# Kernel tuning notes

Measured on AMD Instinct MI355X. Metric: run time of the kernel, lower is better.

The kernel has to match this reference:

```python
import jax, jax.numpy as jnp
import numpy as np

N_NODES = 100000
N_EDGES = 1600000
D_IN = 128
D_HID = 128
D_OUT = 128


def setup_inputs() -> dict:
    key = jax.random.key(0)
    ks = jax.random.split(key, 6)
    node_features = jax.random.normal(ks[0], (N_NODES, D_IN), dtype=jnp.float32)
    edge_index = jax.random.randint(ks[1], (2, N_EDGES), 0, N_NODES, dtype=jnp.int32)
    s1 = 1.0 / np.sqrt(D_IN)
    s2 = 1.0 / np.sqrt(D_HID)
    W1 = jax.random.normal(ks[2], (D_IN, D_HID), dtype=jnp.float32) * s1
    W2 = jax.random.normal(ks[3], (D_HID, D_HID), dtype=jnp.float32) * s2
    W3 = jax.random.normal(ks[4], (D_HID, D_OUT), dtype=jnp.float32) * s2
    b1 = jnp.zeros((D_HID,), dtype=jnp.float32)
    b2 = jnp.zeros((D_HID,), dtype=jnp.float32)
    b3 = jnp.zeros((D_OUT,), dtype=jnp.float32)
    return {"node_features": node_features, "edge_index": edge_index,
            "W1": W1, "b1": b1, "W2": W2, "b2": b2, "W3": W3, "b3": b3}


def _aggregate(x, src, dst, n_nodes):
    # mean over incoming neighbors (by dst), residual add; degree clamped to >=1
    msg = jax.ops.segment_sum(x[src], dst, num_segments=n_nodes)  # [N, D]
    deg = jax.ops.segment_sum(jnp.ones_like(dst, dtype=x.dtype), dst,
                              num_segments=n_nodes)
    deg = jnp.maximum(deg, 1.0)[:, None]
    return x + msg / deg


def reference(node_features, edge_index, W1, b1, W2, b2, W3, b3):
    n_nodes = node_features.shape[0]
    src, dst = edge_index[0], edge_index[1]
    x = _aggregate(node_features, src, dst, n_nodes)
    x = jax.nn.relu(x @ W1 + b1)
    x = _aggregate(x, src, dst, n_nodes)
    x = jax.nn.relu(x @ W2 + b2)
    x = x.mean(axis=0)  # graph readout -> [D_HID]
    return x @ W3 + b3  # [D_OUT]
```

## Files before the change

### kernel.cpp

```cpp
#include <hip/hip_runtime.h>

#define D 128
#define SLOTS 64
#define NB 391
#define NBANK 4
#define SUBCAP 1536
#define BINCAP (NBANK * SUBCAP)
#define BATCH 2048
#define EPB 8
#define CNTSTRIDE 16
#define WPITCH 136

typedef __attribute__((ext_vector_type(8))) short short8;
typedef __attribute__((ext_vector_type(4))) float float4v;

__device__ inline unsigned short f2bf(float f) {
    union { float f; unsigned u; } a; a.f = f;
    unsigned u = a.u;
    return (unsigned short)((u + 0x7fffu + ((u >> 16) & 1u)) >> 16);
}
__device__ inline unsigned packbf(float a, float b) {
    return (unsigned)f2bf(a) | ((unsigned)f2bf(b) << 16);
}
__device__ inline unsigned pack4fp8(float a, float b, float c, float d) {
    int t = __builtin_amdgcn_cvt_pk_fp8_f32(a, b, 0, false);
    t = __builtin_amdgcn_cvt_pk_fp8_f32(c, d, t, true);
    return (unsigned)t;
}
__device__ inline unsigned char pack1fp8(float a) {
    int t = __builtin_amdgcn_cvt_pk_fp8_f32(a, 0.f, 0, false);
    return (unsigned char)(t & 0xff);
}
__device__ inline void acc8fp8(float* acc, uint2 w) {
    auto f0 = __builtin_amdgcn_cvt_pk_f32_fp8(w.x, false);
    auto f1 = __builtin_amdgcn_cvt_pk_f32_fp8(w.x, true);
    auto f2 = __builtin_amdgcn_cvt_pk_f32_fp8(w.y, false);
    auto f3 = __builtin_amdgcn_cvt_pk_f32_fp8(w.y, true);
    acc[0] += f0[0]; acc[1] += f0[1]; acc[2] += f1[0]; acc[3] += f1[1];
    acc[4] += f2[0]; acc[5] += f2[1]; acc[6] += f3[0]; acc[7] += f3[1];
}


__global__ __launch_bounds__(256) void k_head(const int* __restrict__ src,
                                              const int* __restrict__ dst, int nE,
                                              int* __restrict__ gcnt, int* __restrict__ bins,
                                              const float* __restrict__ x,
                                              unsigned char* __restrict__ y8,
                                              unsigned char* __restrict__ h8dummy,
                                              float* __restrict__ colsum,
                                              int n16, int nBatches) {
    __shared__ int hist[512];
    __shared__ int excl[512];
    __shared__ int base[NB];
    __shared__ int stage[BATCH];
    __shared__ int gofs[BATCH];
    __shared__ int waveSum[4];
    int tid = threadIdx.x;

    if (blockIdx.x >= nBatches) {
        int cb = blockIdx.x - nBatches;
        if (cb == 0) {
            if (tid < 128) colsum[tid] = 0.f;
            else if (tid < 136)
                reinterpret_cast<uint4*>(y8)[(size_t)n16 + (tid - 128)] = make_uint4(0, 0, 0, 0);
            else if (tid < 144)
                reinterpret_cast<uint4*>(h8dummy)[tid - 136] = make_uint4(0, 0, 0, 0);
        }
        int i = cb * 256 + tid;
        if (i < n16) {
            const float4* xin = reinterpret_cast<const float4*>(x) + (size_t)i * 4;
            float4 v0 = xin[0], v1 = xin[1], v2 = xin[2], v3 = xin[3];
            uint4 o;
            o.x = pack4fp8(v0.x, v0.y, v0.z, v0.w);
            o.y = pack4fp8(v1.x, v1.y, v1.z, v1.w);
            o.z = pack4fp8(v2.x, v2.y, v2.z, v2.w);
            o.w = pack4fp8(v3.x, v3.y, v3.z, v3.w);
            reinterpret_cast<uint4*>(y8)[i] = o;
        }
        return;
    }

    int start = blockIdx.x * BATCH;
    int cntB = nE - start; if (cntB > BATCH) cntB = BATCH;
    if (cntB <= 0) return;
    int bank = blockIdx.x & (NBANK - 1);

    hist[tid] = 0; hist[tid + 256] = 0;
    __syncthreads();

    int b[EPB], r[EPB], v[EPB];
    #pragma unroll
    for (int i = 0; i < EPB; ++i) {
        int e = start + i * 256 + tid;
        if (e < nE) {
            int d = dst[e];
            b[i] = d >> 8;
            v[i] = (src[e] << 8) | (d & 255);
            r[i] = atomicAdd(&hist[b[i]], 1);
        } else b[i] = -1;
    }
    __syncthreads();

    int e0 = tid * 2, e1 = e0 + 1;
    int h0 = hist[e0], h1v = hist[e1];
    int s = h0 + h1v;
    int lane = tid & 63, w = tid >> 6;
    int sum = s;
    #pragma unroll
    for (int off2 = 1; off2 < 64; off2 <<= 1) {
        int tmp = __shfl_up(sum, off2, 64);
        if (lane >= off2) sum += tmp;
    }
    if (lane == 63) waveSum[w] = sum;
    __syncthreads();
    int wbase = 0;
    if (w > 0) wbase += waveSum[0];
    if (w > 1) wbase += waveSum[1];
    if (w > 2) wbase += waveSum[2];
    int exclPair = wbase + sum - s;
    excl[e0] = exclPair;
    excl[e1] = exclPair + h0;
    if (tid < NB)
        base[tid] = atomicAdd(&gcnt[(tid * NBANK + bank) * CNTSTRIDE], hist[tid]);
    if (tid + 256 < NB)
        base[tid + 256] = atomicAdd(&gcnt[((tid + 256) * NBANK + bank) * CNTSTRIDE], hist[tid + 256]);
    __syncthreads();

    #pragma unroll
    for (int i = 0; i < EPB; ++i) {
        if (b[i] >= 0) {
            int p = excl[b[i]] + r[i];
            int o = base[b[i]] + r[i];
            stage[p] = v[i];
            gofs[p] = (o < SUBCAP) ? (b[i] * BINCAP + bank * SUBCAP + o) : -1;
        }
    }
    __syncthreads();

    #pragma unroll
    for (int i = 0; i < EPB; ++i) {
        int p = i * 256 + tid;
        if (p < cntB) {
            int g = gofs[p];
            if (g >= 0) bins[g] = stage[p];
        }
    }
}


__global__ __launch_bounds__(256) void k_scatter2(const int* __restrict__ gcnt,
                                                  const int* __restrict__ bins,
                                                  int* __restrict__ slots,
                                                  int* __restrict__ deg, int n, int nAll) {
    __shared__ int slotsL[128 * SLOTS];
    __shared__ int cntL[128];
    __shared__ int cnt4s[128];
    int tid = threadIdx.x;
    int bin = blockIdx.x >> 1;
    int half = blockIdx.x & 1;
    if (tid < 128) cntL[tid] = 0;
    __syncthreads();

    #pragma unroll
    for (int k = 0; k < NBANK; ++k) {
        int c = gcnt[(bin * NBANK + k) * CNTSTRIDE]; if (c > SUBCAP) c = SUBCAP;
        const int* eb = bins + (size_t)bin * BINCAP + k * SUBCAP;
        for (int i = tid; i < c; i += 256) {
            int vv = eb[i];
            int dl = vv & 255;
            if ((dl >> 7) == half) {
                int p = atomicAdd(&cntL[dl & 127], 1);
                if (p < SLOTS) slotsL[(dl & 127) * SLOTS + p] = vv >> 8;
            }
        }
    }
    __syncthreads();

    int node0 = bin * 256 + half * 128;
    int remNodes = n - node0;
    if (remNodes > 128) remNodes = 128;
    if (remNodes < 0) remNodes = 0;

    if (tid < remNodes) {
        int dg = cntL[tid]; if (dg > SLOTS) dg = SLOTS;
        int dgr = (dg + 3) & ~3;
        for (int p = dg; p < dgr; ++p) slotsL[tid * SLOTS + p] = nAll;
        deg[node0 + tid] = dg;
        cnt4s[tid] = dgr;
    }
    __syncthreads();

    uint4* gout = reinterpret_cast<uint4*>(slots + (size_t)node0 * SLOTS);
    const uint4* lin = reinterpret_cast<const uint4*>(slotsL);
    int nv = remNodes * (SLOTS / 4);
    for (int i = tid; i < nv; i += 256) {
        int nd = i >> 4, vec = i & 15;
        if ((vec << 2) < cnt4s[nd]) gout[i] = lin[i];
    }
}


__global__ void k_agg(const unsigned char* __restrict__ Xin8,
                      unsigned short* __restrict__ Xout,
                      const int* __restrict__ deg, const int* __restrict__ slots, int n) {
    int t = blockIdx.x * 256 + threadIdx.x;
    int node = t >> 4;
    int lane = t & 15;
    if (node >= n) return;
    int dg = deg[node];
    int cnt4 = (dg + 3) & ~3;
    float acc[8] = {0.f, 0.f, 0.f, 0.f, 0.f, 0.f, 0.f, 0.f};
    const int* sl = slots + (size_t)node * SLOTS;
    for (int j = 0; j < cnt4; j += 4) {
        int4 s4 = *reinterpret_cast<const int4*>(sl + j);
        uint2 w0 = *reinterpret_cast<const uint2*>(Xin8 + (size_t)s4.x * D + lane * 8);
        uint2 w1 = *reinterpret_cast<const uint2*>(Xin8 + (size_t)s4.y * D + lane * 8);
        uint2 w2 = *reinterpret_cast<const uint2*>(Xin8 + (size_t)s4.z * D + lane * 8);
        uint2 w3 = *reinterpret_cast<const uint2*>(Xin8 + (size_t)s4.w * D + lane * 8);
        acc8fp8(acc, w0); acc8fp8(acc, w1); acc8fp8(acc, w2); acc8fp8(acc, w3);
    }
    float inv = 1.0f / (float)(dg > 0 ? dg : 1);
    uint2 s8 = *reinterpret_cast<const uint2*>(Xin8 + (size_t)node * D + lane * 8);
    float self[8] = {0.f, 0.f, 0.f, 0.f, 0.f, 0.f, 0.f, 0.f};
    acc8fp8(self, s8);
    float o[8];
    #pragma unroll
    for (int k = 0; k < 8; ++k) o[k] = self[k] + acc[k] * inv;
    uint4 ov;
    ov.x = packbf(o[0], o[1]); ov.y = packbf(o[2], o[3]);
    ov.z = packbf(o[4], o[5]); ov.w = packbf(o[6], o[7]);
    reinterpret_cast<uint4*>(Xout + (size_t)node * D)[lane] = ov;
}


__global__ __launch_bounds__(256) void k_gemm(const unsigned short* __restrict__ X,
                                              const float* __restrict__ W,
                                              const float* __restrict__ bias,
                                              unsigned char* __restrict__ Y8,
                                              float* __restrict__ colsum,
                                              int n, int mode) {
    __shared__ unsigned short Wt[128 * WPITCH];
    __shared__ float cs[128];
    int tid = threadIdx.x;
    int wave = tid >> 6, L = tid & 63;
    int m16 = L & 15, g = L >> 4;

    #pragma unroll
    for (int i = 0; i < 8; ++i) {
        int p = i * 256 + tid;
        int col = p & 127, kg = p >> 7;
        unsigned pk[4];
        #pragma unroll
        for (int h = 0; h < 4; ++h) {
            float w0 = W[(kg * 8 + 2 * h + 0) * 128 + col];
            float w1 = W[(kg * 8 + 2 * h + 1) * 128 + col];
            pk[h] = packbf(w0, w1);
        }
        *reinterpret_cast<uint4*>(&Wt[col * WPITCH + kg * 8]) =
            make_uint4(pk[0], pk[1], pk[2], pk[3]);
    }
    if (mode && tid < 128) cs[tid] = 0.f;
    __syncthreads();

    int row0 = blockIdx.x * 128 + wave * 32;
    float4v zero4 = {0.f, 0.f, 0.f, 0.f};
    float4v acc[2][8];
    #pragma unroll
    for (int rt = 0; rt < 2; ++rt)
        #pragma unroll
        for (int ct = 0; ct < 8; ++ct) acc[rt][ct] = zero4;

    #pragma unroll
    for (int q = 0; q < 4; ++q) {
        int k0 = q * 32;
        short8 a[2];
        #pragma unroll
        for (int rt = 0; rt < 2; ++rt) {
            int row = row0 + rt * 16 + m16;
            short8 af = {0, 0, 0, 0, 0, 0, 0, 0};
            if (row < n)
                af = *reinterpret_cast<const short8*>(X + (size_t)row * D + k0 + g * 8);
            a[rt] = af;
        }
        #pragma unroll
        for (int ct = 0; ct < 8; ++ct) {
            short8 b = *reinterpret_cast<const short8*>(&Wt[(ct * 16 + m16) * WPITCH + k0 + g * 8]);
            acc[0][ct] = __builtin_amdgcn_mfma_f32_16x16x32_bf16(a[0], b, acc[0][ct], 0, 0, 0);
            acc[1][ct] = __builtin_amdgcn_mfma_f32_16x16x32_bf16(a[1], b, acc[1][ct], 0, 0, 0);
        }
    }

    float bj[8];
    #pragma unroll
    for (int ct = 0; ct < 8; ++ct) bj[ct] = bias[ct * 16 + m16];

    if (mode == 0) {
        #pragma unroll
        for (int rt = 0; rt < 2; ++rt)
            #pragma unroll
            for (int i = 0; i < 4; ++i) {
                int row = row0 + rt * 16 + g * 4 + i;
                if (row < n) {
                    #pragma unroll
                    for (int ct = 0; ct < 8; ++ct) {
                        float v = fmaxf(acc[rt][ct][i] + bj[ct], 0.f);
                        Y8[(size_t)row * D + ct * 16 + m16] = pack1fp8(v);
                    }
                }
            }
    } else {
        float csv[8] = {0.f, 0.f, 0.f, 0.f, 0.f, 0.f, 0.f, 0.f};
        #pragma unroll
        for (int rt = 0; rt < 2; ++rt)
            #pragma unroll
            for (int i = 0; i < 4; ++i) {
                int row = row0 + rt * 16 + g * 4 + i;
                if (row < n) {
                    #pragma unroll
                    for (int ct = 0; ct < 8; ++ct)
                        csv[ct] += fmaxf(acc[rt][ct][i] + bj[ct], 0.f);
                }
            }
        #pragma unroll
        for (int ct = 0; ct < 8; ++ct) atomicAdd(&cs[ct * 16 + m16], csv[ct]);
        __syncthreads();
        if (tid < 128) atomicAdd(&colsum[tid], cs[tid]);
    }
}


__global__ void k_final(const float* __restrict__ colsum, const float* __restrict__ W3,
                        const float* __restrict__ b3, float* __restrict__ out, float invN) {
    int j = threadIdx.x;
    float acc = b3[j];
    #pragma unroll 8
    for (int k = 0; k < D; ++k)
        acc += colsum[k] * invN * W3[k * D + j];
    out[j] = acc;
}


extern "C" void kernel_launch(void* const* d_in, const int* in_sizes, int n_in,
                              void* d_out, int out_size, void* d_ws, size_t ws_size,
                              hipStream_t stream) {
    const float* nf = (const float*)d_in[0];
    const int*   ei = (const int*)d_in[1];
    const float* W1 = (const float*)d_in[2];
    const float* b1 = (const float*)d_in[3];
    const float* W2 = (const float*)d_in[4];
    const float* b2 = (const float*)d_in[5];
    const float* W3 = (const float*)d_in[6];
    const float* b3 = (const float*)d_in[7];
    float* out = (float*)d_out;

    int n  = in_sizes[0] / D;
    int nE = in_sizes[1] / 2;
    const int* src = ei;
    const int* dst = ei + nE;

    int nBins = (n + 255) / 256;
    int nBatches = (nE + BATCH - 1) / BATCH;
    int n16 = n * (D / 16);

    char* ws = (char*)d_ws;
    size_t off = 0;
    auto alloc = [&](size_t bytes) -> void* {
        off = (off + 255) & ~(size_t)255;
        void* p = ws + off;
        off += bytes;
        return p;
    };
    int* gcnt  = (int*)alloc((size_t)nBins * NBANK * CNTSTRIDE * 4);
    int* bins  = (int*)alloc((size_t)nBins * BINCAP * 4);
    int* slots = (int*)alloc((size_t)nBins * 256 * SLOTS * 4);
    int* deg   = (int*)alloc((size_t)n * 4);
    unsigned char*  x8  = (unsigned char*) alloc((size_t)(n + 1) * D);
    unsigned short* t16 = (unsigned short*)alloc((size_t)n * D * 2);
    unsigned char*  h8  = (unsigned char*) alloc((size_t)(n + 1) * D);
    float* colsum = (float*)alloc(128 * 4);

    hipMemsetAsync(gcnt, 0, (size_t)nBins * NBANK * CNTSTRIDE * 4, stream);

    int gC = (n16 + 255) / 256;
    int gA = (n * 16 + 255) / 256;
    int gG = (n + 127) / 128;

    k_head<<<nBatches + gC, 256, 0, stream>>>(src, dst, nE, gcnt, bins,
                                              nf, x8, h8 + (size_t)n * D,
                                              colsum, n16, nBatches);
    k_scatter2<<<nBins * 2, 256, 0, stream>>>(gcnt, bins, slots, deg, n, n);

    k_agg<<<gA, 256, 0, stream>>>(x8, t16, deg, slots, n);
    k_gemm<<<gG, 256, 0, stream>>>(t16, W1, b1, h8, (float*)nullptr, n, 0);
    k_agg<<<gA, 256, 0, stream>>>(h8, t16, deg, slots, n);
    k_gemm<<<gG, 256, 0, stream>>>(t16, W2, b2, (unsigned char*)nullptr, colsum, n, 1);
    k_final<<<1, 128, 0, stream>>>(colsum, W3, b3, out, 1.0f / (float)n);
}
```

Baseline: 257.1 us.

## Fuse neighbor aggregation into GEMM kernel via shared-memory staging

Replaces the separate aggregation and GEMM kernels with one kernel that gathers and mean-aggregates neighbors for a 128-row tile into LDS as bf16, then runs the MFMA GEMM from LDS. This removes the global bf16 intermediate write/read and two kernel launches per layer. In exchange, each thread now processes several nodes serially (two at a time), so gather parallelism per launch drops, and the doubled LDS use may reduce occupancy for the latency-bound random gathers.

```diff
diff --git a/kernel.cpp b/kernel.cpp
--- a/kernel.cpp
+++ b/kernel.cpp
@@ -200,50 +200,21 @@
 }
 
 
-__global__ void k_agg(const unsigned char* __restrict__ Xin8,
-                      unsigned short* __restrict__ Xout,
-                      const int* __restrict__ deg, const int* __restrict__ slots, int n) {
-    int t = blockIdx.x * 256 + threadIdx.x;
-    int node = t >> 4;
-    int lane = t & 15;
-    if (node >= n) return;
-    int dg = deg[node];
-    int cnt4 = (dg + 3) & ~3;
-    float acc[8] = {0.f, 0.f, 0.f, 0.f, 0.f, 0.f, 0.f, 0.f};
-    const int* sl = slots + (size_t)node * SLOTS;
-    for (int j = 0; j < cnt4; j += 4) {
-        int4 s4 = *reinterpret_cast<const int4*>(sl + j);
-        uint2 w0 = *reinterpret_cast<const uint2*>(Xin8 + (size_t)s4.x * D + lane * 8);
-        uint2 w1 = *reinterpret_cast<const uint2*>(Xin8 + (size_t)s4.y * D + lane * 8);
-        uint2 w2 = *reinterpret_cast<const uint2*>(Xin8 + (size_t)s4.z * D + lane * 8);
-        uint2 w3 = *reinterpret_cast<const uint2*>(Xin8 + (size_t)s4.w * D + lane * 8);
-        acc8fp8(acc, w0); acc8fp8(acc, w1); acc8fp8(acc, w2); acc8fp8(acc, w3);
-    }
-    float inv = 1.0f / (float)(dg > 0 ? dg : 1);
-    uint2 s8 = *reinterpret_cast<const uint2*>(Xin8 + (size_t)node * D + lane * 8);
-    float self[8] = {0.f, 0.f, 0.f, 0.f, 0.f, 0.f, 0.f, 0.f};
-    acc8fp8(self, s8);
-    float o[8];
-    #pragma unroll
-    for (int k = 0; k < 8; ++k) o[k] = self[k] + acc[k] * inv;
-    uint4 ov;
-    ov.x = packbf(o[0], o[1]); ov.y = packbf(o[2], o[3]);
-    ov.z = packbf(o[4], o[5]); ov.w = packbf(o[6], o[7]);
-    reinterpret_cast<uint4*>(Xout + (size_t)node * D)[lane] = ov;
-}
-
-
-__global__ __launch_bounds__(256) void k_gemm(const unsigned short* __restrict__ X,
-                                              const float* __restrict__ W,
-                                              const float* __restrict__ bias,
-                                              unsigned char* __restrict__ Y8,
-                                              float* __restrict__ colsum,
-                                              int n, int mode) {
+__global__ __launch_bounds__(256) void k_aggemm(const unsigned char* __restrict__ Xin8,
+                                                const float* __restrict__ W,
+                                                const float* __restrict__ bias,
+                                                unsigned char* __restrict__ Y8,
+                                                float* __restrict__ colsum,
+                                                const int* __restrict__ deg,
+                                                const int* __restrict__ slots,
+                                                int n, int mode) {
     __shared__ unsigned short Wt[128 * WPITCH];
+    __shared__ unsigned short At[128 * WPITCH];
     __shared__ float cs[128];
     int tid = threadIdx.x;
     int wave = tid >> 6, L = tid & 63;
     int m16 = L & 15, g = L >> 4;
+    int row0blk = blockIdx.x * 128;
 
     #pragma unroll
     for (int i = 0; i < 8; ++i) {
@@ -260,9 +231,67 @@
             make_uint4(pk[0], pk[1], pk[2], pk[3]);
     }
     if (mode && tid < 128) cs[tid] = 0.f;
-    __syncthreads();
-
-    int row0 = blockIdx.x * 128 + wave * 32;
+
+    int lane16 = tid & 15;
+    int grp = tid >> 4;
+    #pragma unroll 1
+    for (int p = 0; p < 8; p += 2) {
+        int nlA = p * 16 + grp;
+        int nlB = nlA + 16;
+        int nodeA = row0blk + nlA, nodeB = row0blk + nlB;
+        float accA[8] = {0.f, 0.f, 0.f, 0.f, 0.f, 0.f, 0.f, 0.f};
+        float accB[8] = {0.f, 0.f, 0.f, 0.f, 0.f, 0.f, 0.f, 0.f};
+        int cA = 0, cB = 0, dgA = 0, dgB = 0;
+        const int *slA = slots, *slB = slots;
+        if (nodeA < n) { dgA = deg[nodeA]; cA = (dgA + 3) & ~3; slA = slots + (size_t)nodeA * SLOTS; }
+        if (nodeB < n) { dgB = deg[nodeB]; cB = (dgB + 3) & ~3; slB = slots + (size_t)nodeB * SLOTS; }
+        int cM = cA > cB ? cA : cB;
+        for (int j = 0; j < cM; j += 4) {
+            if (j < cA) {
+                int4 s4 = *reinterpret_cast<const int4*>(slA + j);
+                uint2 w0 = *reinterpret_cast<const uint2*>(Xin8 + (size_t)s4.x * D + lane16 * 8);
+                uint2 w1 = *reinterpret_cast<const uint2*>(Xin8 + (size_t)s4.y * D + lane16 * 8);
+                uint2 w2 = *reinterpret_cast<const uint2*>(Xin8 + (size_t)s4.z * D + lane16 * 8);
+                uint2 w3 = *reinterpret_cast<const uint2*>(Xin8 + (size_t)s4.w * D + lane16 * 8);
+                acc8fp8(accA, w0); acc8fp8(accA, w1); acc8fp8(accA, w2); acc8fp8(accA, w3);
+            }
+            if (j < cB) {
+                int4 s4 = *reinterpret_cast<const int4*>(slB + j);
+                uint2 w0 = *reinterpret_cast<const uint2*>(Xin8 + (size_t)s4.x * D + lane16 * 8);
+                uint2 w1 = *reinterpret_cast<const uint2*>(Xin8 + (size_t)s4.y * D + lane16 * 8);
+                uint2 w2 = *reinterpret_cast<const uint2*>(Xin8 + (size_t)s4.z * D + lane16 * 8);
+                uint2 w3 = *reinterpret_cast<const uint2*>(Xin8 + (size_t)s4.w * D + lane16 * 8);
+                acc8fp8(accB, w0); acc8fp8(accB, w1); acc8fp8(accB, w2); acc8fp8(accB, w3);
+            }
+        }
+        if (nodeA < n) {
+            float inv = 1.0f / (float)(dgA > 0 ? dgA : 1);
+            uint2 s8 = *reinterpret_cast<const uint2*>(Xin8 + (size_t)nodeA * D + lane16 * 8);
+            float self[8] = {0.f, 0.f, 0.f, 0.f, 0.f, 0.f, 0.f, 0.f};
+            acc8fp8(self, s8);
+            uint4 ov;
+            ov.x = packbf(self[0] + accA[0] * inv, self[1] + accA[1] * inv);
+            ov.y = packbf(self[2] + accA[2] * inv, self[3] + accA[3] * inv);
+            ov.z = packbf(self[4] + accA[4] * inv, self[5] + accA[5] * inv);
+            ov.w = packbf(self[6] + accA[6] * inv, self[7] + accA[7] * inv);
+            *reinterpret_cast<uint4*>(&At[nlA * WPITCH + lane16 * 8]) = ov;
+        }
+        if (nodeB < n) {
+            float inv = 1.0f / (float)(dgB > 0 ? dgB : 1);
+            uint2 s8 = *reinterpret_cast<const uint2*>(Xin8 + (size_t)nodeB * D + lane16 * 8);
+            float self[8] = {0.f, 0.f, 0.f, 0.f, 0.f, 0.f, 0.f, 0.f};
+            acc8fp8(self, s8);
+            uint4 ov;
+            ov.x = packbf(self[0] + accB[0] * inv, self[1] + accB[1] * inv);
+            ov.y = packbf(self[2] + accB[2] * inv, self[3] + accB[3] * inv);
+            ov.z = packbf(self[4] + accB[4] * inv, self[5] + accB[5] * inv);
+            ov.w = packbf(self[6] + accB[6] * inv, self[7] + accB[7] * inv);
+            *reinterpret_cast<uint4*>(&At[nlB * WPITCH + lane16 * 8]) = ov;
+        }
+    }
+    __syncthreads();
+
+    int row0 = row0blk + wave * 32;
     float4v zero4 = {0.f, 0.f, 0.f, 0.f};
     float4v acc[2][8];
     #pragma unroll
@@ -275,13 +304,9 @@
         int k0 = q * 32;
         short8 a[2];
         #pragma unroll
-        for (int rt = 0; rt < 2; ++rt) {
-            int row = row0 + rt * 16 + m16;
-            short8 af = {0, 0, 0, 0, 0, 0, 0, 0};
-            if (row < n)
-                af = *reinterpret_cast<const short8*>(X + (size_t)row * D + k0 + g * 8);
-            a[rt] = af;
-        }
+        for (int rt = 0; rt < 2; ++rt)
+            a[rt] = *reinterpret_cast<const short8*>(
+                &At[(wave * 32 + rt * 16 + m16) * WPITCH + k0 + g * 8]);
         #pragma unroll
         for (int ct = 0; ct < 8; ++ct) {
             short8 b = *reinterpret_cast<const short8*>(&Wt[(ct * 16 + m16) * WPITCH + k0 + g * 8]);
@@ -375,14 +400,12 @@
     int* slots = (int*)alloc((size_t)nBins * 256 * SLOTS * 4);
     int* deg   = (int*)alloc((size_t)n * 4);
     unsigned char*  x8  = (unsigned char*) alloc((size_t)(n + 1) * D);
-    unsigned short* t16 = (unsigned short*)alloc((size_t)n * D * 2);
     unsigned char*  h8  = (unsigned char*) alloc((size_t)(n + 1) * D);
     float* colsum = (float*)alloc(128 * 4);
 
     hipMemsetAsync(gcnt, 0, (size_t)nBins * NBANK * CNTSTRIDE * 4, stream);
 
     int gC = (n16 + 255) / 256;
-    int gA = (n * 16 + 255) / 256;
     int gG = (n + 127) / 128;
 
     k_head<<<nBatches + gC, 256, 0, stream>>>(src, dst, nE, gcnt, bins,
@@ -390,9 +413,7 @@
                                               colsum, n16, nBatches);
     k_scatter2<<<nBins * 2, 256, 0, stream>>>(gcnt, bins, slots, deg, n, n);
 
-    k_agg<<<gA, 256, 0, stream>>>(x8, t16, deg, slots, n);
-    k_gemm<<<gG, 256, 0, stream>>>(t16, W1, b1, h8, (float*)nullptr, n, 0);
-    k_agg<<<gA, 256, 0, stream>>>(h8, t16, deg, slots, n);
-    k_gemm<<<gG, 256, 0, stream>>>(t16, W2, b2, (unsigned char*)nullptr, colsum, n, 1);
+    k_aggemm<<<gG, 256, 0, stream>>>(x8, W1, b1, h8, (float*)nullptr, deg, slots, n, 0);
+    k_aggemm<<<gG, 256, 0, stream>>>(h8, W2, b2, (unsigned char*)nullptr, colsum, deg, slots, n, 1);
     k_final<<<1, 128, 0, stream>>>(colsum, W3, b3, out, 1.0f / (float)n);
 }
```

After: 327.5 us. 27.4% more time.
